# Kernel optimization log

Measured on AMD Instinct MI355X. Metric: run time of the kernel, lower is better.

## Reference

```python
import jax, jax.numpy as jnp
import numpy as np


def setup_inputs() -> dict:
    key = jax.random.key(0)
    k1, k2, k3, k4, k5 = jax.random.split(key, 5)
    B, N, M, D = 4096, 2048, 2048, 9
    return {
        "x": jax.random.normal(k1, (B, N), dtype=jnp.float32),
        "eternal_weights": jax.random.normal(k2, (D, N, M), dtype=jnp.float32),
        "eternal_biases": jax.random.normal(k3, (M,), dtype=jnp.float32),
        "classical_weights": jax.random.normal(k4, (N, M), dtype=jnp.float32),
        "classical_biases": jax.random.normal(k5, (M,), dtype=jnp.float32),
    }


def _eternal_probs(eternal_weights, n, m):
    # The gate matrix is cos*I - sin*P + sin*P^T with P the circular shift,
    # so (gate @ s)[i] = cos*s[i] - sin*s[(i+1)%n] + sin*s[(i-1)%n].
    # Vectorize over all m output units at once: state is [m, n].
    state0 = jnp.full((m, n), 1.0 / np.sqrt(n), dtype=eternal_weights.dtype)
    angles = eternal_weights[:, :m, :3]  # [D, m, 3] -- weights[depth, j, 0/1/2]

    def gate(state, angle):  # angle: [m]
        c = jnp.cos(angle)[:, None]
        s = jnp.sin(angle)[:, None]
        return c * state - s * jnp.roll(state, -1, axis=1) + s * jnp.roll(state, 1, axis=1)

    def step(state, ang):  # ang: [m, 3] -- consciousness, intelligence, wisdom
        state = gate(state, ang[:, 0])
        state = gate(state, ang[:, 1])
        state = gate(state, ang[:, 2])
        return state, None

    state, _ = jax.lax.scan(step, state0, angles)
    return jnp.abs(state[:, 0]) ** 2  # [m]


def reference(x, eternal_weights, eternal_biases, classical_weights, classical_biases):
    # eternal_biases exists as a parameter in the original module but is unused in forward.
    n = x.shape[1]
    m = classical_weights.shape[1]
    classical = x @ classical_weights + classical_biases  # [B, m]
    probs = _eternal_probs(eternal_weights, n, m)  # [m], identical for every batch row
    return jnp.tanh(classical + probs[None, :])
```

## Files before the change

kernel.cpp:

```cpp
#include <hip/hip_runtime.h>
#include <stdint.h>

static constexpr int MM = 4096;
static constexpr int KK = 2048;
static constexpr int NN = 2048;

typedef float floatx4 __attribute__((ext_vector_type(4)));
typedef __bf16 bf16x8 __attribute__((ext_vector_type(8)));

__device__ __forceinline__ unsigned short bf16_rne(float x) {
  union { float f; uint32_t u; } c; c.f = x;
  uint32_t u = c.u;
  u += 0x7fffu + ((u >> 16) & 1u);
  return (unsigned short)(u >> 16);
}
__device__ __forceinline__ float bf16_as_f32(unsigned short h) {
  union { float f; uint32_t u; } c; c.u = ((uint32_t)h) << 16;
  return c.f;
}

__global__ __launch_bounds__(256) void split_x_kernel(
    const float* __restrict__ in, unsigned short* __restrict__ hi,
    unsigned short* __restrict__ lo, int n4) {
  int idx = blockIdx.x * 256 + threadIdx.x;
  if (idx >= n4) return;
  float4 v = ((const float4*)in)[idx];
  ushort4 h, l;
  float t;
  h.x = bf16_rne(v.x); t = v.x - bf16_as_f32(h.x); l.x = bf16_rne(t);
  h.y = bf16_rne(v.y); t = v.y - bf16_as_f32(h.y); l.y = bf16_rne(t);
  h.z = bf16_rne(v.z); t = v.z - bf16_as_f32(h.z); l.z = bf16_rne(t);
  h.w = bf16_rne(v.w); t = v.w - bf16_as_f32(h.w); l.w = bf16_rne(t);
  ((ushort4*)hi)[idx] = h;
  ((ushort4*)lo)[idx] = l;
}

__global__ __launch_bounds__(256) void wsplit_kernel(
    const float* __restrict__ W, unsigned short* __restrict__ bhi,
    unsigned short* __restrict__ blo) {
  __shared__ float tile[32][33];
  const int tx = threadIdx.x;
  const int ty = threadIdx.y;
  const int n0 = blockIdx.x * 32;
  const int k0 = blockIdx.y * 32;
#pragma unroll
  for (int i = 0; i < 4; i++) {
    int k = k0 + ty * 4 + i;
    tile[ty * 4 + i][tx] = W[(size_t)k * NN + n0 + tx];
  }
  __syncthreads();
#pragma unroll
  for (int i = 0; i < 4; i++) {
    int n = n0 + ty * 4 + i;
    float v = tile[tx][ty * 4 + i];
    unsigned short h = bf16_rne(v);
    float lof = v - bf16_as_f32(h);
    size_t o = (size_t)n * KK + k0 + tx;
    bhi[o] = h;
    blo[o] = bf16_rne(lof);
  }
}

__global__ __launch_bounds__(256) void bias_probs_kernel(
    const float* __restrict__ E, const float* __restrict__ cb,
    float* __restrict__ bias2) {
  int i = blockIdx.x * 256 + threadIdx.x;
  if (i >= NN) return;
  float p = 1.0f / 2048.0f;
#pragma unroll
  for (int d = 0; d < 9; d++) {
    const float* a = E + (size_t)d * (2048 * 2048) + (size_t)i * 2048;
#pragma unroll
    for (int t = 0; t < 3; t++) {
      float c = cosf(a[t]);
      p *= c * c;
    }
  }
  bias2[i] = cb[i] + p;
}

#define GLL(dst, src)                                                        \
  __builtin_amdgcn_global_load_lds(                                          \
      (const __attribute__((address_space(1))) void*)(src),                  \
      (__attribute__((address_space(3))) void*)(dst), 16, 0, 0)

__global__ __launch_bounds__(256, 2) void gemm_tanh_kernel(
    const unsigned short* __restrict__ Ahi, const unsigned short* __restrict__ Alo,
    const unsigned short* __restrict__ Bhi, const unsigned short* __restrict__ Blo,
    const float* __restrict__ bias2, float* __restrict__ out) {
  __shared__ __align__(16) unsigned short sA[2][128 * 32];
  __shared__ __align__(16) unsigned short sB[2][128 * 32];

  const int tid = threadIdx.x;
  const int lane = tid & 63;
  const int wave = tid >> 6;
  const int wm = (wave >> 1) * 64;
  const int wn = (wave & 1) * 64;
  const int bm = blockIdx.y * 128;
  const int bn = blockIdx.x * 128;

  const int srow = tid >> 2;
  const int scol = (tid & 3) * 8;
  const size_t a_base = (size_t)(bm + srow) * KK + scol;
  const size_t b_base = (size_t)(bn + srow) * KK + scol;
  const int lds_off = tid * 8;

  const int fm = lane & 15;
  const int fk = (lane >> 4) * 8;

  floatx4 acc[4][4];
#pragma unroll
  for (int i = 0; i < 4; i++)
#pragma unroll
    for (int j = 0; j < 4; j++) acc[i][j] = {0.f, 0.f, 0.f, 0.f};

  for (int k0 = 0; k0 < KK; k0 += 32) {
    GLL(&sA[0][lds_off],        Ahi + a_base + k0);
    GLL(&sA[0][lds_off + 2048], Ahi + a_base + k0 + (size_t)64 * KK);
    GLL(&sA[1][lds_off],        Alo + a_base + k0);
    GLL(&sA[1][lds_off + 2048], Alo + a_base + k0 + (size_t)64 * KK);
    GLL(&sB[0][lds_off],        Bhi + b_base + k0);
    GLL(&sB[0][lds_off + 2048], Bhi + b_base + k0 + (size_t)64 * KK);
    GLL(&sB[1][lds_off],        Blo + b_base + k0);
    GLL(&sB[1][lds_off + 2048], Blo + b_base + k0 + (size_t)64 * KK);
    __syncthreads();

    bf16x8 fa[2][4], fb[2][4];
#pragma unroll
    for (int t = 0; t < 4; t++) {
      int ao = (wm + t * 16 + fm) * 32 + fk;
      fa[0][t] = *(const bf16x8*)(&sA[0][ao]);
      fa[1][t] = *(const bf16x8*)(&sA[1][ao]);
      int bo = (wn + t * 16 + fm) * 32 + fk;
      fb[0][t] = *(const bf16x8*)(&sB[0][bo]);
      fb[1][t] = *(const bf16x8*)(&sB[1][bo]);
    }
#pragma unroll
    for (int i = 0; i < 4; i++)
#pragma unroll
      for (int j = 0; j < 4; j++) {
        acc[i][j] = __builtin_amdgcn_mfma_f32_16x16x32_bf16(fa[0][i], fb[0][j], acc[i][j], 0, 0, 0);
        acc[i][j] = __builtin_amdgcn_mfma_f32_16x16x32_bf16(fa[0][i], fb[1][j], acc[i][j], 0, 0, 0);
        acc[i][j] = __builtin_amdgcn_mfma_f32_16x16x32_bf16(fa[1][i], fb[0][j], acc[i][j], 0, 0, 0);
      }
    __syncthreads();
  }

  const int cr = (lane >> 4) * 4;
  const int cc = lane & 15;
#pragma unroll
  for (int j = 0; j < 4; j++) {
    int col = bn + wn + j * 16 + cc;
    float b2 = bias2[col];
#pragma unroll
    for (int i = 0; i < 4; i++) {
      int row0 = bm + wm + i * 16 + cr;
      floatx4 a = acc[i][j];
#pragma unroll
      for (int r = 0; r < 4; r++) {
        out[(size_t)(row0 + r) * NN + col] = tanhf(a[r] + b2);
      }
    }
  }
}

__global__ __launch_bounds__(256) void fallback_gemm(
    const float* __restrict__ x, const float* __restrict__ E,
    const float* __restrict__ W, const float* __restrict__ cb,
    float* __restrict__ out) {
  __shared__ float sA[16][16];
  __shared__ float sB[16][17];
  __shared__ float sbias[16];
  const int tx = threadIdx.x, ty = threadIdx.y;
  const int row = blockIdx.y * 16 + ty;
  const int col = blockIdx.x * 16 + tx;
  if (ty == 0) {
    float p = 1.0f / 2048.0f;
    for (int d = 0; d < 9; d++) {
      const float* a = E + (size_t)d * (2048 * 2048) + (size_t)col * 2048;
      for (int t = 0; t < 3; t++) { float c = cosf(a[t]); p *= c * c; }
    }
    sbias[tx] = p + cb[col];
  }
  float acc = 0.f;
  for (int k0 = 0; k0 < KK; k0 += 16) {
    __syncthreads();
    sA[ty][tx] = x[(size_t)row * KK + k0 + tx];
    sB[ty][tx] = W[(size_t)(k0 + ty) * NN + col];
    __syncthreads();
#pragma unroll
    for (int kk = 0; kk < 16; kk++) acc += sA[ty][kk] * sB[kk][tx];
  }
  out[(size_t)row * NN + col] = tanhf(acc + sbias[tx]);
}

extern "C" void kernel_launch(void* const* d_in, const int* in_sizes, int n_in,
                              void* d_out, int out_size, void* d_ws, size_t ws_size,
                              hipStream_t stream) {
  const float* x  = (const float*)d_in[0];
  const float* E  = (const float*)d_in[1];
  const float* W  = (const float*)d_in[3];
  const float* cb = (const float*)d_in[4];
  float* out = (float*)d_out;

  const size_t MB = 1024 * 1024;
  const size_t need = 48 * MB + NN * sizeof(float);
  if (ws_size < need) {
    fallback_gemm<<<dim3(NN / 16, MM / 16), dim3(16, 16), 0, stream>>>(x, E, W, cb, out);
    return;
  }

  char* ws = (char*)d_ws;
  unsigned short* Ahi = (unsigned short*)(ws);
  unsigned short* Alo = (unsigned short*)(ws + 16 * MB);
  unsigned short* Bhi = (unsigned short*)(ws + 32 * MB);
  unsigned short* Blo = (unsigned short*)(ws + 40 * MB);
  float* bias2 = (float*)(ws + 48 * MB);

  const int n4 = MM * KK / 4;
  split_x_kernel<<<dim3((n4 + 255) / 256), dim3(256), 0, stream>>>(x, Ahi, Alo, n4);
  wsplit_kernel<<<dim3(NN / 32, KK / 32), dim3(32, 8), 0, stream>>>(W, Bhi, Blo);
  bias_probs_kernel<<<dim3((NN + 255) / 256), dim3(256), 0, stream>>>(E, cb, bias2);
  gemm_tanh_kernel<<<dim3(NN / 128, MM / 128), dim3(256), 0, stream>>>(
      Ahi, Alo, Bhi, Blo, bias2, out);
}
```

Measured before the change: 341.6 us.

## Swizzle bf16 split layout to avoid LDS bank conflicts and shrink GEMM N-tile

```diff
diff --git a/kernel.cpp b/kernel.cpp
--- a/kernel.cpp
+++ b/kernel.cpp
@@ -7,6 +7,7 @@
 
 typedef float floatx4 __attribute__((ext_vector_type(4)));
 typedef __bf16 bf16x8 __attribute__((ext_vector_type(8)));
+typedef unsigned short u16x8 __attribute__((ext_vector_type(8)));
 
 __device__ __forceinline__ unsigned short bf16_rne(float x) {
   union { float f; uint32_t u; } c; c.f = x;
@@ -19,45 +20,69 @@
   return c.f;
 }
 
+
 __global__ __launch_bounds__(256) void split_x_kernel(
     const float* __restrict__ in, unsigned short* __restrict__ hi,
-    unsigned short* __restrict__ lo, int n4) {
+    unsigned short* __restrict__ lo, int nchunks) {
   int idx = blockIdx.x * 256 + threadIdx.x;
-  if (idx >= n4) return;
-  float4 v = ((const float4*)in)[idx];
-  ushort4 h, l;
-  float t;
-  h.x = bf16_rne(v.x); t = v.x - bf16_as_f32(h.x); l.x = bf16_rne(t);
-  h.y = bf16_rne(v.y); t = v.y - bf16_as_f32(h.y); l.y = bf16_rne(t);
-  h.z = bf16_rne(v.z); t = v.z - bf16_as_f32(h.z); l.z = bf16_rne(t);
-  h.w = bf16_rne(v.w); t = v.w - bf16_as_f32(h.w); l.w = bf16_rne(t);
-  ((ushort4*)hi)[idx] = h;
-  ((ushort4*)lo)[idx] = l;
+  if (idx >= nchunks) return;
+  int row = idx >> 8;
+  int ck = idx & 255;
+  int p = ck >> 2;
+  int c = ck & 3;
+  const float4* s = (const float4*)(in + (size_t)row * KK + ck * 8);
+  float4 v0 = s[0], v1 = s[1];
+  float vv[8] = {v0.x, v0.y, v0.z, v0.w, v1.x, v1.y, v1.z, v1.w};
+  u16x8 h, l;
+#pragma unroll
+  for (int e = 0; e < 8; e++) {
+    unsigned short hh = bf16_rne(vv[e]);
+    h[e] = hh;
+    l[e] = bf16_rne(vv[e] - bf16_as_f32(hh));
+  }
+  size_t dst = (size_t)row * KK + p * 32 + ((c + (row >> 1)) & 3) * 8;
+  *(u16x8*)(hi + dst) = h;
+  *(u16x8*)(lo + dst) = l;
 }
 
 __global__ __launch_bounds__(256) void wsplit_kernel(
     const float* __restrict__ W, unsigned short* __restrict__ bhi,
     unsigned short* __restrict__ blo) {
-  __shared__ float tile[32][33];
-  const int tx = threadIdx.x;
-  const int ty = threadIdx.y;
-  const int n0 = blockIdx.x * 32;
-  const int k0 = blockIdx.y * 32;
+  __shared__ float tile[64][65];
+  const int tid = threadIdx.x;
+  const int n0 = blockIdx.x * 64;
+  const int k0 = blockIdx.y * 64;
 #pragma unroll
   for (int i = 0; i < 4; i++) {
-    int k = k0 + ty * 4 + i;
-    tile[ty * 4 + i][tx] = W[(size_t)k * NN + n0 + tx];
+    int t = tid + i * 256;
+    int kr = t >> 4;
+    int nc = (t & 15) * 4;
+    const float4 v = *(const float4*)(W + (size_t)(k0 + kr) * NN + n0 + nc);
+    tile[nc + 0][kr] = v.x;
+    tile[nc + 1][kr] = v.y;
+    tile[nc + 2][kr] = v.z;
+    tile[nc + 3][kr] = v.w;
   }
   __syncthreads();
-#pragma unroll
-  for (int i = 0; i < 4; i++) {
-    int n = n0 + ty * 4 + i;
-    float v = tile[tx][ty * 4 + i];
-    unsigned short h = bf16_rne(v);
-    float lof = v - bf16_as_f32(h);
-    size_t o = (size_t)n * KK + k0 + tx;
-    bhi[o] = h;
-    blo[o] = bf16_rne(lof);
+  const int nl = tid >> 2;
+  const int q = tid & 3;
+  const int n = n0 + nl;
+#pragma unroll
+  for (int cc = 0; cc < 2; cc++) {
+    int c_loc = q * 2 + cc;
+    int p_loc = c_loc >> 2;
+    int kc = c_loc & 3;
+    u16x8 h, l;
+#pragma unroll
+    for (int e = 0; e < 8; e++) {
+      float v = tile[nl][c_loc * 8 + e];
+      unsigned short hh = bf16_rne(v);
+      h[e] = hh;
+      l[e] = bf16_rne(v - bf16_as_f32(hh));
+    }
+    size_t dst = (size_t)n * KK + (k0 + p_loc * 32) + ((kc + (n >> 1)) & 3) * 8;
+    *(u16x8*)(bhi + dst) = h;
+    *(u16x8*)(blo + dst) = l;
   }
 }
 
@@ -84,35 +109,33 @@
       (const __attribute__((address_space(1))) void*)(src),                  \
       (__attribute__((address_space(3))) void*)(dst), 16, 0, 0)
 
-__global__ __launch_bounds__(256, 2) void gemm_tanh_kernel(
+__global__ __launch_bounds__(256, 4) void gemm_tanh_kernel(
     const unsigned short* __restrict__ Ahi, const unsigned short* __restrict__ Alo,
     const unsigned short* __restrict__ Bhi, const unsigned short* __restrict__ Blo,
     const float* __restrict__ bias2, float* __restrict__ out) {
   __shared__ __align__(16) unsigned short sA[2][128 * 32];
-  __shared__ __align__(16) unsigned short sB[2][128 * 32];
+  __shared__ __align__(16) unsigned short sB[2][64 * 32];
 
   const int tid = threadIdx.x;
   const int lane = tid & 63;
   const int wave = tid >> 6;
   const int wm = (wave >> 1) * 64;
-  const int wn = (wave & 1) * 64;
+  const int wn = (wave & 1) * 32;
   const int bm = blockIdx.y * 128;
-  const int bn = blockIdx.x * 128;
-
-  const int srow = tid >> 2;
-  const int scol = (tid & 3) * 8;
-  const size_t a_base = (size_t)(bm + srow) * KK + scol;
-  const size_t b_base = (size_t)(bn + srow) * KK + scol;
+  const int bn = blockIdx.x * 64;
+
+  const size_t a_base = (size_t)(bm + (tid >> 2)) * KK + (tid & 3) * 8;
+  const size_t b_base = (size_t)(bn + (tid >> 2)) * KK + (tid & 3) * 8;
   const int lds_off = tid * 8;
 
   const int fm = lane & 15;
-  const int fk = (lane >> 4) * 8;
-
-  floatx4 acc[4][4];
+  const int kq = lane >> 4;
+
+  floatx4 acc[4][2];
 #pragma unroll
   for (int i = 0; i < 4; i++)
 #pragma unroll
-    for (int j = 0; j < 4; j++) acc[i][j] = {0.f, 0.f, 0.f, 0.f};
+    for (int j = 0; j < 2; j++) acc[i][j] = {0.f, 0.f, 0.f, 0.f};
 
   for (int k0 = 0; k0 < KK; k0 += 32) {
     GLL(&sA[0][lds_off],        Ahi + a_base + k0);
@@ -120,25 +143,28 @@
     GLL(&sA[1][lds_off],        Alo + a_base + k0);
     GLL(&sA[1][lds_off + 2048], Alo + a_base + k0 + (size_t)64 * KK);
     GLL(&sB[0][lds_off],        Bhi + b_base + k0);
-    GLL(&sB[0][lds_off + 2048], Bhi + b_base + k0 + (size_t)64 * KK);
     GLL(&sB[1][lds_off],        Blo + b_base + k0);
-    GLL(&sB[1][lds_off + 2048], Blo + b_base + k0 + (size_t)64 * KK);
-    __syncthreads();
-
-    bf16x8 fa[2][4], fb[2][4];
+    __syncthreads();
+
+    bf16x8 fa[2][4], fb[2][2];
 #pragma unroll
     for (int t = 0; t < 4; t++) {
-      int ao = (wm + t * 16 + fm) * 32 + fk;
+      int rowA = wm + t * 16 + fm;
+      int ao = rowA * 32 + ((kq + (rowA >> 1)) & 3) * 8;
       fa[0][t] = *(const bf16x8*)(&sA[0][ao]);
       fa[1][t] = *(const bf16x8*)(&sA[1][ao]);
-      int bo = (wn + t * 16 + fm) * 32 + fk;
-      fb[0][t] = *(const bf16x8*)(&sB[0][bo]);
-      fb[1][t] = *(const bf16x8*)(&sB[1][bo]);
+    }
+#pragma unroll
+    for (int j = 0; j < 2; j++) {
+      int rowB = wn + j * 16 + fm;
+      int bo = rowB * 32 + ((kq + (rowB >> 1)) & 3) * 8;
+      fb[0][j] = *(const bf16x8*)(&sB[0][bo]);
+      fb[1][j] = *(const bf16x8*)(&sB[1][bo]);
     }
 #pragma unroll
     for (int i = 0; i < 4; i++)
 #pragma unroll
-      for (int j = 0; j < 4; j++) {
+      for (int j = 0; j < 2; j++) {
         acc[i][j] = __builtin_amdgcn_mfma_f32_16x16x32_bf16(fa[0][i], fb[0][j], acc[i][j], 0, 0, 0);
         acc[i][j] = __builtin_amdgcn_mfma_f32_16x16x32_bf16(fa[0][i], fb[1][j], acc[i][j], 0, 0, 0);
         acc[i][j] = __builtin_amdgcn_mfma_f32_16x16x32_bf16(fa[1][i], fb[0][j], acc[i][j], 0, 0, 0);
@@ -149,7 +175,7 @@
   const int cr = (lane >> 4) * 4;
   const int cc = lane & 15;
 #pragma unroll
-  for (int j = 0; j < 4; j++) {
+  for (int j = 0; j < 2; j++) {
     int col = bn + wn + j * 16 + cc;
     float b2 = bias2[col];
 #pragma unroll
@@ -217,10 +243,10 @@
   unsigned short* Blo = (unsigned short*)(ws + 40 * MB);
   float* bias2 = (float*)(ws + 48 * MB);
 
-  const int n4 = MM * KK / 4;
-  split_x_kernel<<<dim3((n4 + 255) / 256), dim3(256), 0, stream>>>(x, Ahi, Alo, n4);
-  wsplit_kernel<<<dim3(NN / 32, KK / 32), dim3(32, 8), 0, stream>>>(W, Bhi, Blo);
+  const int nchunks = MM * KK / 8;
+  split_x_kernel<<<dim3(nchunks / 256), dim3(256), 0, stream>>>(x, Ahi, Alo, nchunks);
+  wsplit_kernel<<<dim3(NN / 64, KK / 64), dim3(256), 0, stream>>>(W, Bhi, Blo);
   bias_probs_kernel<<<dim3((NN + 255) / 256), dim3(256), 0, stream>>>(E, cb, bias2);
-  gemm_tanh_kernel<<<dim3(NN / 128, MM / 128), dim3(256), 0, stream>>>(
+  gemm_tanh_kernel<<<dim3(NN / 64, MM / 128), dim3(256), 0, stream>>>(
       Ahi, Alo, Bhi, Blo, bias2, out);
 }
```

Result: slower. 369.5 us (+8.2%).
